# Kernel optimization log

Hardware: AMD Instinct MI355X
Metric: run time of the kernel (lower is better)

## Reference

```python
import jax, jax.numpy as jnp
import numpy as np

EPS = 1e-3
LOG2PI = float(np.log(2.0 * np.pi))

# dims
B, Z, Y, T, D = 32768, 256, 32, 64, 4  # batch, z_dim, y_dim, n_types, type_dim


def setup_inputs() -> dict:
    key = jax.random.key(0)
    ks = jax.random.split(key, 8)
    z = jax.random.normal(ks[0], (B, Z), dtype=jnp.float32)
    batch_x = jax.random.normal(ks[1], (B, T, D), dtype=jnp.float32)
    miss_list = jax.random.randint(ks[2], (B, T), 0, 2, dtype=jnp.int32)  # 1=observed, 0=missing
    data_mean = jax.random.normal(ks[3], (T, D), dtype=jnp.float32)
    data_var = jax.random.uniform(ks[4], (T, D), dtype=jnp.float32, minval=0.5, maxval=1.5)
    # weights init N(0, 0.005) as in the torch module; biases zero
    Wy = jax.random.normal(ks[5], (T * Y, Z), dtype=jnp.float32) * 0.005
    by = jnp.zeros((T * Y,), dtype=jnp.float32)
    Wm = jax.random.normal(ks[6], (T, D, Y), dtype=jnp.float32) * 0.005
    bm = jnp.zeros((T, D), dtype=jnp.float32)
    Wv = jax.random.normal(ks[7], (T, D, Y), dtype=jnp.float32) * 0.005
    bv = jnp.zeros((T, D), dtype=jnp.float32)
    return {"z": z, "batch_x": batch_x, "miss_list": miss_list,
            "data_mean": data_mean, "data_var": data_var,
            "Wy": Wy, "by": by, "Wm": Wm, "bm": bm, "Wv": Wv, "bv": bv}


def reference(z, batch_x, miss_list, data_mean, data_var, Wy, by, Wm, bm, Wv, bv):
    # y_layer: z -> [B, T*Y], grouped into per-type gamma slices [B, T, Y]
    y = z @ Wy.T + by
    gamma = y.reshape(y.shape[0], T, Y)

    mask = miss_list.astype(gamma.dtype)            # [B, T], 1=observed
    m3 = mask[:, :, None]                           # [B, T, 1]

    # per-type tiny linears (dynamic_partition + Linear + dynamic_stitch).
    # Numerically: same linear on all rows; missing rows are under no_grad,
    # realized here as stop_gradient on the missing partition.
    lin_m = jnp.einsum('bty,tdy->btd', gamma, Wm) + bm   # [B, T, D]
    lin_v = jnp.einsum('bty,tdy->btd', gamma, Wv) + bv
    est_mean = m3 * lin_m + (1.0 - m3) * jax.lax.stop_gradient(lin_m)
    est_var_raw = m3 * lin_v + (1.0 - m3) * jax.lax.stop_gradient(lin_v)

    # loglik_real: softplus variance, denormalize with data mean/var
    dvar = jnp.clip(data_var, EPS)
    est_var = jnp.clip(jax.nn.softplus(est_var_raw), EPS, 1e20)
    mean_x = jnp.sqrt(dvar) * est_mean + data_mean       # [B, T, D]
    var_x = dvar * est_var                               # [B, T, D]

    log_p = -0.5 * jnp.sum((batch_x - mean_x) ** 2 / var_x + jnp.log(var_x) + LOG2PI, axis=-1)  # [B, T]
    log_p_x = log_p * mask
    log_p_x_missing = log_p * (1.0 - mask)
    return (log_p_x, log_p_x_missing, mean_x, var_x)
```

## Files before the change

kernel.cpp:

```cpp
#include <hip/hip_runtime.h>


#define Bsz   32768
#define Tsz   64
#define Dsz   4
#define Ysz   32
#define Zsz   256
#define Nsz   512
#define BTtot (Bsz * Tsz)
#define EPS_  1e-3f
#define LOG2PI_ 1.8378770664093453f

#define BM       32
#define NT       256
#define ASTRIDE  264
#define LSTRIDE  520

typedef __attribute__((ext_vector_type(4))) float  f32x4;
typedef __attribute__((ext_vector_type(8))) short  short8;
typedef __attribute__((ext_vector_type(2))) unsigned int uint2v;

static __device__ __forceinline__ unsigned short f2bf(float f) {
    unsigned int u = __float_as_uint(f);
    return (unsigned short)((u + 0x7fffu + ((u >> 16) & 1u)) >> 16);
}
static __device__ __forceinline__ float bf2f(unsigned short h) {
    return __uint_as_float(((unsigned int)h) << 16);
}

__global__ __launch_bounds__(256)
void hidec_prep(const float* __restrict__ Wy, const float* __restrict__ by,
                const float* __restrict__ Wm, const float* __restrict__ bm,
                const float* __restrict__ Wv, const float* __restrict__ bv,
                unsigned short* __restrict__ weff, float* __restrict__ beff) {
    __shared__ float Ml[8][Ysz];
    __shared__ float byl[Ysz];
    const int t   = blockIdx.x;
    const int tid = threadIdx.x;
    {
        int j = tid >> 5, y = tid & 31;
        const float* src = (j < 4) ? Wm : Wv;
        Ml[j][y] = src[(t * Dsz + (j & 3)) * Ysz + y];
    }
    if (tid < Ysz) byl[tid] = by[t * Ysz + tid];
    __syncthreads();

    const int k = tid;
    const int kk = k >> 5, q = (k >> 3) & 3, je = k & 7;
    float wy[Ysz];
#pragma unroll
    for (int y = 0; y < Ysz; ++y)
        wy[y] = Wy[(size_t)(t * Ysz + y) * Zsz + k];
#pragma unroll
    for (int j = 0; j < 8; ++j) {
        float acc = 0.f;
#pragma unroll
        for (int y = 0; y < Ysz; ++y) acc = fmaf(Ml[j][y], wy[y], acc);
        int n   = t * 8 + j;
        int tau = n >> 4, c = n & 15;
        weff[((((tau * 8 + kk) * 4 + q) * 16 + c) * 8) + je] = f2bf(acc);
    }
    if (tid < 8) {
        int d = tid & 3;
        float s = ((tid < 4) ? bm : bv)[t * Dsz + d];
        for (int y = 0; y < Ysz; ++y) s = fmaf(byl[y], Ml[tid][y], s);
        beff[t * 8 + tid] = s;
    }
}

__global__ __launch_bounds__(NT, 4)
void hidec_main(const float* __restrict__ z, const float* __restrict__ bx,
                const int* __restrict__ miss, const float* __restrict__ dmean,
                const float* __restrict__ dvarp, const unsigned short* __restrict__ weff,
                const float* __restrict__ beff, float* __restrict__ out) {
    __shared__ unsigned short buf[BM * LSTRIDE];
    __shared__ float4 sqA[Tsz], dmA[Tsz], dcA[Tsz];
    __shared__ float  sldv[Tsz];
    __shared__ float  beffL[Nsz];

    const int tid  = threadIdx.x;
    const long row0 = (long)blockIdx.x * BM;

    if (tid < Tsz) {
        float4 dv4 = *(const float4*)(dvarp + tid * 4);
        float4 dm4 = *(const float4*)(dmean + tid * 4);
        float d0 = fmaxf(dv4.x, EPS_), d1 = fmaxf(dv4.y, EPS_);
        float d2 = fmaxf(dv4.z, EPS_), d3 = fmaxf(dv4.w, EPS_);
        sqA[tid] = (float4){sqrtf(d0), sqrtf(d1), sqrtf(d2), sqrtf(d3)};
        dmA[tid] = dm4;
        dcA[tid] = (float4){d0, d1, d2, d3};
        sldv[tid] = __logf(d0) + __logf(d1) + __logf(d2) + __logf(d3);
    }
    beffL[tid]       = beff[tid];
    beffL[tid + 256] = beff[tid + 256];

    unsigned short* a_lds = buf;
#pragma unroll
    for (int i = 0; i < 8; ++i) {
        int idx4 = tid + i * NT;
        int r  = idx4 >> 6;
        int c4 = idx4 & 63;
        float4 v = *(const float4*)(z + (row0 + r) * Zsz + c4 * 4);
        uint2v p;
        p.x = (unsigned)f2bf(v.x) | ((unsigned)f2bf(v.y) << 16);
        p.y = (unsigned)f2bf(v.z) | ((unsigned)f2bf(v.w) << 16);
        *(uint2v*)&a_lds[r * ASTRIDE + c4 * 4] = p;
    }
    __syncthreads();

    const int lane = tid & 63;
    const int w    = tid >> 6;
    const int c    = lane & 15;
    const int q    = lane >> 4;

    f32x4 acc[16];
#pragma unroll
    for (int i = 0; i < 16; ++i) acc[i] = (f32x4){0.f, 0.f, 0.f, 0.f};

    const unsigned short* wp = weff + (size_t)w * 32768 + lane * 8;

#pragma unroll
    for (int kk = 0; kk < 8; ++kk) {
        short8 a0 = *(const short8*)&a_lds[(0 * 16 + c) * ASTRIDE + kk * 32 + q * 8];
        short8 a1 = *(const short8*)&a_lds[(1 * 16 + c) * ASTRIDE + kk * 32 + q * 8];
#pragma unroll
        for (int ti = 0; ti < 8; ++ti) {
            short8 b = *(const short8*)(wp + (size_t)(ti * 8 + kk) * 512);
            acc[ti * 2 + 0] = __builtin_amdgcn_mfma_f32_16x16x32_bf16(a0, b, acc[ti * 2 + 0], 0, 0, 0);
            acc[ti * 2 + 1] = __builtin_amdgcn_mfma_f32_16x16x32_bf16(a1, b, acc[ti * 2 + 1], 0, 0, 0);
        }
    }
    __syncthreads();

    unsigned short* lin = buf;
#pragma unroll
    for (int ti = 0; ti < 8; ++ti) {
        int n  = (w * 8 + ti) * 16 + c;
        float bb = beffL[n];
        int t  = n >> 3;
        int jj = n & 7;
#pragma unroll
        for (int rt = 0; rt < 2; ++rt) {
#pragma unroll
            for (int reg = 0; reg < 4; ++reg) {
                int rl = rt * 16 + q * 4 + reg;
                lin[rl * LSTRIDE + t * 8 + jj] = f2bf(acc[ti * 2 + rt][reg] + bb);
            }
        }
    }
    __syncthreads();

#pragma unroll
    for (int pp = 0; pp < 8; ++pp) {
        int task = pp * NT + tid;
        int t  = task & 63;
        int rl = task >> 6;
        long bt = (row0 + rl) * Tsz + t;

        short8 l8 = *(const short8*)&lin[rl * LSTRIDE + t * 8];
        float lm[4], lv[4];
#pragma unroll
        for (int d = 0; d < 4; ++d) {
            lm[d] = bf2f((unsigned short)l8[d]);
            lv[d] = bf2f((unsigned short)l8[4 + d]);
        }

        float4 x4  = *(const float4*)(bx + bt * 4);
        float4 sq4 = sqA[t];
        float4 dm4 = dmA[t];
        float4 dc4 = dcA[t];
        float xa[4]  = {x4.x,  x4.y,  x4.z,  x4.w};
        float sqa[4] = {sq4.x, sq4.y, sq4.z, sq4.w};
        float dma[4] = {dm4.x, dm4.y, dm4.z, dm4.w};
        float dca[4] = {dc4.x, dc4.y, dc4.z, dc4.w};

        float mean_o[4], var_o[4];
        float s = sldv[t];
        float evp = 1.f;
#pragma unroll
        for (int d = 0; d < 4; ++d) {
            float mean = fmaf(sqa[d], lm[d], dma[d]);
            float v    = lv[d];
            float sp   = fmaxf(v, 0.f) + __logf(1.f + __expf(-fabsf(v)));
            float ev   = fminf(fmaxf(sp, EPS_), 1e20f);
            float var  = dca[d] * ev;
            float diff = xa[d] - mean;
            s = fmaf(diff * diff, __builtin_amdgcn_rcpf(var), s);
            evp *= ev;
            mean_o[d] = mean;
            var_o[d]  = var;
        }
        s += __logf(evp);
        float logp = -0.5f * (s + 4.f * LOG2PI_);
        float mk = (float)miss[bt];

        float lx = logp * mk;
        out[bt]         = lx;
        out[BTtot + bt] = logp - lx;

        *(float4*)(out + 2L * BTtot + bt * 4) =
            (float4){mean_o[0], mean_o[1], mean_o[2], mean_o[3]};
        *(float4*)(out + 6L * BTtot + bt * 4) =
            (float4){var_o[0], var_o[1], var_o[2], var_o[3]};
    }
}

extern "C" void kernel_launch(void* const* d_in, const int* in_sizes, int n_in,
                              void* d_out, int out_size, void* d_ws, size_t ws_size,
                              hipStream_t stream) {
    const float* z     = (const float*)d_in[0];
    const float* bx    = (const float*)d_in[1];
    const int*   miss  = (const int*)d_in[2];
    const float* dmean = (const float*)d_in[3];
    const float* dvar  = (const float*)d_in[4];
    const float* Wy    = (const float*)d_in[5];
    const float* by    = (const float*)d_in[6];
    const float* Wm    = (const float*)d_in[7];
    const float* bm    = (const float*)d_in[8];
    const float* Wv    = (const float*)d_in[9];
    const float* bv    = (const float*)d_in[10];
    float* out = (float*)d_out;

    unsigned short* weff = (unsigned short*)d_ws;
    float* beff = (float*)((char*)d_ws + (size_t)Nsz * Zsz * 2);

    hidec_prep<<<Tsz, Zsz, 0, stream>>>(Wy, by, Wm, bm, Wv, bv, weff, beff);
    hidec_main<<<Bsz / BM, NT, 0, stream>>>(z, bx, miss, dmean, dvar, weff, beff, out);
}
```

Measured before the change: 184.3 us.

## Split fused GEMM+epilogue into separate GEMM and elementwise kernels via workspace

```diff
diff --git a/kernel.cpp b/kernel.cpp
--- a/kernel.cpp
+++ b/kernel.cpp
@@ -11,8 +11,8 @@
 #define EPS_  1e-3f
 #define LOG2PI_ 1.8378770664093453f
 
-#define BM       32
-#define NT       256
+#define BMg      64
+#define NTg      512
 #define ASTRIDE  264
 #define LSTRIDE  520
 
@@ -68,19 +68,97 @@
     }
 }
 
-__global__ __launch_bounds__(NT, 4)
-void hidec_main(const float* __restrict__ z, const float* __restrict__ bx,
-                const int* __restrict__ miss, const float* __restrict__ dmean,
-                const float* __restrict__ dvarp, const unsigned short* __restrict__ weff,
-                const float* __restrict__ beff, float* __restrict__ out) {
-    __shared__ unsigned short buf[BM * LSTRIDE];
+__global__ __launch_bounds__(NTg, 4)
+void hidec_gemm(const float* __restrict__ z, const unsigned short* __restrict__ weff,
+                const float* __restrict__ beff, unsigned short* __restrict__ lin) {
+    __shared__ unsigned short buf[32 * LSTRIDE > BMg * ASTRIDE ? 32 * LSTRIDE
+                                                               : BMg * ASTRIDE];
+    __shared__ float beffL[Nsz];
+
+    const int tid  = threadIdx.x;
+    const long row0 = (long)blockIdx.x * BMg;
+
+    beffL[tid] = beff[tid];
+
+    unsigned short* a_lds = buf;
+#pragma unroll
+    for (int i = 0; i < 8; ++i) {
+        int idx4 = tid + i * NTg;
+        int r  = idx4 >> 6;
+        int c4 = idx4 & 63;
+        float4 v = *(const float4*)(z + (row0 + r) * Zsz + c4 * 4);
+        uint2v p;
+        p.x = (unsigned)f2bf(v.x) | ((unsigned)f2bf(v.y) << 16);
+        p.y = (unsigned)f2bf(v.z) | ((unsigned)f2bf(v.w) << 16);
+        *(uint2v*)&a_lds[r * ASTRIDE + c4 * 4] = p;
+    }
+    __syncthreads();
+
+    const int lane = tid & 63;
+    const int w    = tid >> 6;
+    const int c    = lane & 15;
+    const int q    = lane >> 4;
+
+    f32x4 acc[16];
+#pragma unroll
+    for (int i = 0; i < 16; ++i) acc[i] = (f32x4){0.f, 0.f, 0.f, 0.f};
+
+    const unsigned short* wp = weff + (size_t)w * 16384 + lane * 8;
+
+#pragma unroll
+    for (int kk = 0; kk < 8; ++kk) {
+        short8 a0 = *(const short8*)&a_lds[(0 * 16 + c) * ASTRIDE + kk * 32 + q * 8];
+        short8 a1 = *(const short8*)&a_lds[(1 * 16 + c) * ASTRIDE + kk * 32 + q * 8];
+        short8 a2 = *(const short8*)&a_lds[(2 * 16 + c) * ASTRIDE + kk * 32 + q * 8];
+        short8 a3 = *(const short8*)&a_lds[(3 * 16 + c) * ASTRIDE + kk * 32 + q * 8];
+#pragma unroll
+        for (int ti = 0; ti < 4; ++ti) {
+            short8 b = *(const short8*)(wp + (size_t)(ti * 8 + kk) * 512);
+            acc[ti * 4 + 0] = __builtin_amdgcn_mfma_f32_16x16x32_bf16(a0, b, acc[ti * 4 + 0], 0, 0, 0);
+            acc[ti * 4 + 1] = __builtin_amdgcn_mfma_f32_16x16x32_bf16(a1, b, acc[ti * 4 + 1], 0, 0, 0);
+            acc[ti * 4 + 2] = __builtin_amdgcn_mfma_f32_16x16x32_bf16(a2, b, acc[ti * 4 + 2], 0, 0, 0);
+            acc[ti * 4 + 3] = __builtin_amdgcn_mfma_f32_16x16x32_bf16(a3, b, acc[ti * 4 + 3], 0, 0, 0);
+        }
+    }
+    __syncthreads();
+
+    unsigned short* lbuf = buf;
+#pragma unroll
+    for (int ch = 0; ch < 2; ++ch) {
+#pragma unroll
+        for (int ti = 0; ti < 4; ++ti) {
+            int n  = (w * 4 + ti) * 16 + c;
+            float bb = beffL[n];
+#pragma unroll
+            for (int rh = 0; rh < 2; ++rh) {
+                int rt = ch * 2 + rh;
+#pragma unroll
+                for (int reg = 0; reg < 4; ++reg) {
+                    int rl = rh * 16 + q * 4 + reg;
+                    lbuf[rl * LSTRIDE + n] = f2bf(acc[ti * 4 + rt][reg] + bb);
+                }
+            }
+        }
+        __syncthreads();
+#pragma unroll
+        for (int pp = 0; pp < 4; ++pp) {
+            int task = pp * NTg + tid;
+            int rl = task >> 6;
+            int g  = task & 63;
+            *(short8*)(lin + ((size_t)(row0 + ch * 32 + rl)) * Nsz + g * 8) =
+                *(const short8*)&lbuf[rl * LSTRIDE + g * 8];
+        }
+        __syncthreads();
+    }
+}
+
+__global__ __launch_bounds__(256)
+void hidec_epi(const unsigned short* __restrict__ lin, const float* __restrict__ bx,
+               const int* __restrict__ miss, const float* __restrict__ dmean,
+               const float* __restrict__ dvarp, float* __restrict__ out) {
     __shared__ float4 sqA[Tsz], dmA[Tsz], dcA[Tsz];
     __shared__ float  sldv[Tsz];
-    __shared__ float  beffL[Nsz];
-
-    const int tid  = threadIdx.x;
-    const long row0 = (long)blockIdx.x * BM;
-
+    const int tid = threadIdx.x;
     if (tid < Tsz) {
         float4 dv4 = *(const float4*)(dvarp + tid * 4);
         float4 dm4 = *(const float4*)(dmean + tid * 4);
@@ -91,73 +169,15 @@
         dcA[tid] = (float4){d0, d1, d2, d3};
         sldv[tid] = __logf(d0) + __logf(d1) + __logf(d2) + __logf(d3);
     }
-    beffL[tid]       = beff[tid];
-    beffL[tid + 256] = beff[tid + 256];
-
-    unsigned short* a_lds = buf;
-#pragma unroll
-    for (int i = 0; i < 8; ++i) {
-        int idx4 = tid + i * NT;
-        int r  = idx4 >> 6;
-        int c4 = idx4 & 63;
-        float4 v = *(const float4*)(z + (row0 + r) * Zsz + c4 * 4);
-        uint2v p;
-        p.x = (unsigned)f2bf(v.x) | ((unsigned)f2bf(v.y) << 16);
-        p.y = (unsigned)f2bf(v.z) | ((unsigned)f2bf(v.w) << 16);
-        *(uint2v*)&a_lds[r * ASTRIDE + c4 * 4] = p;
-    }
-    __syncthreads();
-
-    const int lane = tid & 63;
-    const int w    = tid >> 6;
-    const int c    = lane & 15;
-    const int q    = lane >> 4;
-
-    f32x4 acc[16];
-#pragma unroll
-    for (int i = 0; i < 16; ++i) acc[i] = (f32x4){0.f, 0.f, 0.f, 0.f};
-
-    const unsigned short* wp = weff + (size_t)w * 32768 + lane * 8;
-
-#pragma unroll
-    for (int kk = 0; kk < 8; ++kk) {
-        short8 a0 = *(const short8*)&a_lds[(0 * 16 + c) * ASTRIDE + kk * 32 + q * 8];
-        short8 a1 = *(const short8*)&a_lds[(1 * 16 + c) * ASTRIDE + kk * 32 + q * 8];
-#pragma unroll
-        for (int ti = 0; ti < 8; ++ti) {
-            short8 b = *(const short8*)(wp + (size_t)(ti * 8 + kk) * 512);
-            acc[ti * 2 + 0] = __builtin_amdgcn_mfma_f32_16x16x32_bf16(a0, b, acc[ti * 2 + 0], 0, 0, 0);
-            acc[ti * 2 + 1] = __builtin_amdgcn_mfma_f32_16x16x32_bf16(a1, b, acc[ti * 2 + 1], 0, 0, 0);
-        }
-    }
-    __syncthreads();
-
-    unsigned short* lin = buf;
-#pragma unroll
-    for (int ti = 0; ti < 8; ++ti) {
-        int n  = (w * 8 + ti) * 16 + c;
-        float bb = beffL[n];
-        int t  = n >> 3;
-        int jj = n & 7;
-#pragma unroll
-        for (int rt = 0; rt < 2; ++rt) {
-#pragma unroll
-            for (int reg = 0; reg < 4; ++reg) {
-                int rl = rt * 16 + q * 4 + reg;
-                lin[rl * LSTRIDE + t * 8 + jj] = f2bf(acc[ti * 2 + rt][reg] + bb);
-            }
-        }
-    }
-    __syncthreads();
-
-#pragma unroll
-    for (int pp = 0; pp < 8; ++pp) {
-        int task = pp * NT + tid;
-        int t  = task & 63;
-        int rl = task >> 6;
-        long bt = (row0 + rl) * Tsz + t;
-
-        short8 l8 = *(const short8*)&lin[rl * LSTRIDE + t * 8];
+    __syncthreads();
+
+    const size_t base = (size_t)blockIdx.x * 1024 + tid;
+#pragma unroll
+    for (int pp = 0; pp < 4; ++pp) {
+        size_t bt = base + (size_t)pp * 256;
+        int t = (int)(bt & 63);
+
+        short8 l8 = *(const short8*)(lin + bt * 8);
         float lm[4], lv[4];
 #pragma unroll
         for (int d = 0; d < 4; ++d) {
@@ -222,8 +242,10 @@
     float* out = (float*)d_out;
 
     unsigned short* weff = (unsigned short*)d_ws;
-    float* beff = (float*)((char*)d_ws + (size_t)Nsz * Zsz * 2);
+    float* beff = (float*)((char*)d_ws + 262144);
+    unsigned short* lin = (unsigned short*)((char*)d_ws + 264192);
 
     hidec_prep<<<Tsz, Zsz, 0, stream>>>(Wy, by, Wm, bm, Wv, bv, weff, beff);
-    hidec_main<<<Bsz / BM, NT, 0, stream>>>(z, bx, miss, dmean, dvar, weff, beff, out);
-}
+    hidec_gemm<<<Bsz / BMg, NTg, 0, stream>>>(z, weff, beff, lin);
+    hidec_epi<<<BTtot / 1024, 256, 0, stream>>>(lin, bx, miss, dmean, dvar, out);
+}
```

Result: no change. 184.9 us (+0.3%).

## Split output columns across block pairs with 64-row tiles and 512 threads

Applied to the files above, without the earlier changes.

```diff
diff --git a/kernel.cpp b/kernel.cpp
--- a/kernel.cpp
+++ b/kernel.cpp
@@ -11,10 +11,11 @@
 #define EPS_  1e-3f
 #define LOG2PI_ 1.8378770664093453f
 
-#define BM       32
-#define NT       256
+#define BM       64
+#define NH       256
+#define NT       512
 #define ASTRIDE  264
-#define LSTRIDE  520
+#define LPAD     264
 
 typedef __attribute__((ext_vector_type(4))) float  f32x4;
 typedef __attribute__((ext_vector_type(8))) short  short8;
@@ -68,22 +69,25 @@
     }
 }
 
-__global__ __launch_bounds__(NT, 4)
+__global__ __launch_bounds__(NT, 6)
 void hidec_main(const float* __restrict__ z, const float* __restrict__ bx,
                 const int* __restrict__ miss, const float* __restrict__ dmean,
                 const float* __restrict__ dvarp, const unsigned short* __restrict__ weff,
                 const float* __restrict__ beff, float* __restrict__ out) {
-    __shared__ unsigned short buf[BM * LSTRIDE];
-    __shared__ float4 sqA[Tsz], dmA[Tsz], dcA[Tsz];
-    __shared__ float  sldv[Tsz];
-    __shared__ float  beffL[Nsz];
-
-    const int tid  = threadIdx.x;
-    const long row0 = (long)blockIdx.x * BM;
-
-    if (tid < Tsz) {
-        float4 dv4 = *(const float4*)(dvarp + tid * 4);
-        float4 dm4 = *(const float4*)(dmean + tid * 4);
+    __shared__ unsigned short buf[BM * ASTRIDE];
+    __shared__ float4 sqA[32], dmA[32], dcA[32];
+    __shared__ float  sldv[32];
+    __shared__ float  beffL[NH];
+
+    const int tid   = threadIdx.x;
+    const int thalf = (blockIdx.x & 1) * 32;
+    const int nbase = (blockIdx.x & 1) * NH;
+    const long row0 = (long)(blockIdx.x >> 1) * BM;
+
+    if (tid < 32) {
+        int t = thalf + tid;
+        float4 dv4 = *(const float4*)(dvarp + t * 4);
+        float4 dm4 = *(const float4*)(dmean + t * 4);
         float d0 = fmaxf(dv4.x, EPS_), d1 = fmaxf(dv4.y, EPS_);
         float d2 = fmaxf(dv4.z, EPS_), d3 = fmaxf(dv4.w, EPS_);
         sqA[tid] = (float4){sqrtf(d0), sqrtf(d1), sqrtf(d2), sqrtf(d3)};
@@ -91,8 +95,7 @@
         dcA[tid] = (float4){d0, d1, d2, d3};
         sldv[tid] = __logf(d0) + __logf(d1) + __logf(d2) + __logf(d3);
     }
-    beffL[tid]       = beff[tid];
-    beffL[tid + 256] = beff[tid + 256];
+    if (tid < NH) beffL[tid] = beff[nbase + tid];
 
     unsigned short* a_lds = buf;
 #pragma unroll
@@ -113,51 +116,57 @@
     const int c    = lane & 15;
     const int q    = lane >> 4;
 
-    f32x4 acc[16];
-#pragma unroll
-    for (int i = 0; i < 16; ++i) acc[i] = (f32x4){0.f, 0.f, 0.f, 0.f};
-
-    const unsigned short* wp = weff + (size_t)w * 32768 + lane * 8;
+    f32x4 acc[8];
+#pragma unroll
+    for (int i = 0; i < 8; ++i) acc[i] = (f32x4){0.f, 0.f, 0.f, 0.f};
+
+    const unsigned short* wp =
+        weff + ((size_t)((nbase >> 4) + w * 2) * 8) * 512 + lane * 8;
 
 #pragma unroll
     for (int kk = 0; kk < 8; ++kk) {
         short8 a0 = *(const short8*)&a_lds[(0 * 16 + c) * ASTRIDE + kk * 32 + q * 8];
         short8 a1 = *(const short8*)&a_lds[(1 * 16 + c) * ASTRIDE + kk * 32 + q * 8];
-#pragma unroll
-        for (int ti = 0; ti < 8; ++ti) {
-            short8 b = *(const short8*)(wp + (size_t)(ti * 8 + kk) * 512);
-            acc[ti * 2 + 0] = __builtin_amdgcn_mfma_f32_16x16x32_bf16(a0, b, acc[ti * 2 + 0], 0, 0, 0);
-            acc[ti * 2 + 1] = __builtin_amdgcn_mfma_f32_16x16x32_bf16(a1, b, acc[ti * 2 + 1], 0, 0, 0);
-        }
+        short8 a2 = *(const short8*)&a_lds[(2 * 16 + c) * ASTRIDE + kk * 32 + q * 8];
+        short8 a3 = *(const short8*)&a_lds[(3 * 16 + c) * ASTRIDE + kk * 32 + q * 8];
+        short8 b0 = *(const short8*)(wp + (size_t)kk * 512);
+        short8 b1 = *(const short8*)(wp + (size_t)kk * 512 + 4096);
+        acc[0] = __builtin_amdgcn_mfma_f32_16x16x32_bf16(a0, b0, acc[0], 0, 0, 0);
+        acc[1] = __builtin_amdgcn_mfma_f32_16x16x32_bf16(a1, b0, acc[1], 0, 0, 0);
+        acc[2] = __builtin_amdgcn_mfma_f32_16x16x32_bf16(a2, b0, acc[2], 0, 0, 0);
+        acc[3] = __builtin_amdgcn_mfma_f32_16x16x32_bf16(a3, b0, acc[3], 0, 0, 0);
+        acc[4] = __builtin_amdgcn_mfma_f32_16x16x32_bf16(a0, b1, acc[4], 0, 0, 0);
+        acc[5] = __builtin_amdgcn_mfma_f32_16x16x32_bf16(a1, b1, acc[5], 0, 0, 0);
+        acc[6] = __builtin_amdgcn_mfma_f32_16x16x32_bf16(a2, b1, acc[6], 0, 0, 0);
+        acc[7] = __builtin_amdgcn_mfma_f32_16x16x32_bf16(a3, b1, acc[7], 0, 0, 0);
     }
     __syncthreads();
 
     unsigned short* lin = buf;
 #pragma unroll
-    for (int ti = 0; ti < 8; ++ti) {
-        int n  = (w * 8 + ti) * 16 + c;
-        float bb = beffL[n];
-        int t  = n >> 3;
-        int jj = n & 7;
-#pragma unroll
-        for (int rt = 0; rt < 2; ++rt) {
+    for (int ti = 0; ti < 2; ++ti) {
+        int n_loc = (w * 2 + ti) * 16 + c;
+        float bb = beffL[n_loc];
+#pragma unroll
+        for (int rt = 0; rt < 4; ++rt) {
 #pragma unroll
             for (int reg = 0; reg < 4; ++reg) {
                 int rl = rt * 16 + q * 4 + reg;
-                lin[rl * LSTRIDE + t * 8 + jj] = f2bf(acc[ti * 2 + rt][reg] + bb);
+                lin[rl * LPAD + n_loc] = f2bf(acc[ti * 4 + rt][reg] + bb);
             }
         }
     }
     __syncthreads();
 
 #pragma unroll
-    for (int pp = 0; pp < 8; ++pp) {
-        int task = pp * NT + tid;
-        int t  = task & 63;
-        int rl = task >> 6;
-        long bt = (row0 + rl) * Tsz + t;
-
-        short8 l8 = *(const short8*)&lin[rl * LSTRIDE + t * 8];
+    for (int pp = 0; pp < 4; ++pp) {
+        int task  = pp * NT + tid;
+        int t_loc = task & 31;
+        int rl    = task >> 5;
+        int t     = thalf + t_loc;
+        long bt   = (row0 + rl) * Tsz + t;
+
+        short8 l8 = *(const short8*)&lin[rl * LPAD + t_loc * 8];
         float lm[4], lv[4];
 #pragma unroll
         for (int d = 0; d < 4; ++d) {
@@ -166,16 +175,16 @@
         }
 
         float4 x4  = *(const float4*)(bx + bt * 4);
-        float4 sq4 = sqA[t];
-        float4 dm4 = dmA[t];
-        float4 dc4 = dcA[t];
+        float4 sq4 = sqA[t_loc];
+        float4 dm4 = dmA[t_loc];
+        float4 dc4 = dcA[t_loc];
         float xa[4]  = {x4.x,  x4.y,  x4.z,  x4.w};
         float sqa[4] = {sq4.x, sq4.y, sq4.z, sq4.w};
         float dma[4] = {dm4.x, dm4.y, dm4.z, dm4.w};
         float dca[4] = {dc4.x, dc4.y, dc4.z, dc4.w};
 
         float mean_o[4], var_o[4];
-        float s = sldv[t];
+        float s = sldv[t_loc];
         float evp = 1.f;
 #pragma unroll
         for (int d = 0; d < 4; ++d) {
@@ -222,8 +231,8 @@
     float* out = (float*)d_out;
 
     unsigned short* weff = (unsigned short*)d_ws;
-    float* beff = (float*)((char*)d_ws + (size_t)Nsz * Zsz * 2);
+    float* beff = (float*)((char*)d_ws + 262144);
 
     hidec_prep<<<Tsz, Zsz, 0, stream>>>(Wy, by, Wm, bm, Wv, bv, weff, beff);
-    hidec_main<<<Bsz / BM, NT, 0, stream>>>(z, bx, miss, dmean, dvar, weff, beff, out);
-}
+    hidec_main<<<(Bsz / BM) * 2, NT, 0, stream>>>(z, bx, miss, dmean, dvar, weff, beff, out);
+}
```

Result: faster. 176.8 us (-4.1%).
